# Kernel optimization log

Measured on AMD Instinct MI355X. Metric: run time of the kernel, lower is better.

Reference implementation:

```python
import jax, jax.numpy as jnp
import numpy as np

D_MODEL = 1024
N_HEADS = 16
HEAD_DIM = D_MODEL // N_HEADS
MAX_LEN = 32768
Q_LEN = 16
START_POS = MAX_LEN - Q_LEN
SCALE = 1.0 / np.sqrt(HEAD_DIM)


def setup_inputs() -> dict:
    key = jax.random.key(0)
    ks = jax.random.split(key, 7)
    xav = np.sqrt(6.0 / (D_MODEL + D_MODEL))  # xavier_uniform bound
    return {
        "query": jax.random.normal(ks[0], (Q_LEN, D_MODEL), dtype=jnp.float32),
        "Wq": jax.random.uniform(ks[1], (D_MODEL, D_MODEL), jnp.float32, -xav, xav),
        "Wk": jax.random.uniform(ks[2], (D_MODEL, D_MODEL), jnp.float32, -xav, xav),
        "Wv": jax.random.uniform(ks[3], (D_MODEL, D_MODEL), jnp.float32, -xav, xav),
        "Wo": jax.random.uniform(ks[4], (D_MODEL, D_MODEL), jnp.float32, -xav, xav),
        "cache_k": jax.random.normal(ks[5], (MAX_LEN, N_HEADS, HEAD_DIM), dtype=jnp.float32),
        "cache_v": jax.random.normal(ks[6], (MAX_LEN, N_HEADS, HEAD_DIM), dtype=jnp.float32),
        "start_pos": START_POS,
    }


def reference(query, Wq, Wk, Wv, Wo, cache_k, cache_v, start_pos):
    S = query.shape[0]
    # QKV projections (nn.Linear: y = x @ W.T), reshape to [S, H, hd]
    Q = (query @ Wq.T).reshape(S, N_HEADS, HEAD_DIM)
    K = (query @ Wk.T).reshape(S, N_HEADS, HEAD_DIM)
    V = (query @ Wv.T).reshape(S, N_HEADS, HEAD_DIM)
    # KV-cache update: write new K/V at start_pos, attend over [0, start_pos+S)
    T = start_pos + S  # cached_seq_len (static python int)
    cached_K = jax.lax.dynamic_update_slice(cache_k, K, (start_pos, 0, 0))[:T]
    cached_V = jax.lax.dynamic_update_slice(cache_v, V, (start_pos, 0, 0))[:T]
    # scores: [H, S, T]
    scores = jnp.einsum("shd,thd->hst", Q, cached_K) * jnp.float32(SCALE)
    if T > S:
        # mask key pos j > query row i + start_pos (triu with diagonal=start_pos+1)
        row = jnp.arange(S)[:, None]
        col = jnp.arange(T)[None, :]
        scores = jnp.where(col > row + start_pos, jnp.float32(-jnp.inf), scores)
    attn = jax.nn.softmax(scores, axis=-1)
    out = jnp.einsum("hst,thd->shd", attn, cached_V).reshape(S, D_MODEL)
    output = out @ Wo.T
    return output, K, V
```

## Files before the change

### kernel.cpp

```cpp
#include <hip/hip_runtime.h>

#define D      1024
#define H      16
#define HD     64
#define SP     32752
#define TT     32768
#define SCALE  0.125f
#define NC     128
#define CHUNK  256
#define PSTR   260

__device__ __forceinline__ float4 ldg4(const float* p){ return *reinterpret_cast<const float4*>(p); }
__device__ __forceinline__ void   stg4(float* p, float4 v){ *reinterpret_cast<float4*>(p) = v; }

__device__ __forceinline__ float gemm16_val(const float* __restrict__ x,
                                            const float* __restrict__ W,
                                            int ochunk, int* o_out, int* li_out)
{
    const int t  = threadIdx.x;
    const int o  = ochunk * 16 + (t >> 4);
    const int ds = (t & 15) << 6;

    float4 wv[16];
    const float* wp = W + (size_t)o * D + ds;
    #pragma unroll
    for (int d4 = 0; d4 < 16; ++d4) wv[d4] = ldg4(wp + d4 * 4);

    float a[16];
    #pragma unroll
    for (int i = 0; i < 16; ++i) {
        const float* xp = x + (size_t)i * D + ds;
        float s = 0.f;
        #pragma unroll
        for (int d4 = 0; d4 < 16; ++d4) {
            float4 xv = ldg4(xp + d4 * 4);
            s += wv[d4].x * xv.x + wv[d4].y * xv.y + wv[d4].z * xv.z + wv[d4].w * xv.w;
        }
        a[i] = s;
    }
    #pragma unroll
    for (int off = 8; off >= 1; off >>= 1) {
        #pragma unroll
        for (int i = 0; i < 16; ++i) a[i] += __shfl_xor(a[i], off, 16);
    }
    const int li = t & 15;
    float v = a[0];
    #pragma unroll
    for (int i = 1; i < 16; ++i) v = (li == i) ? a[i] : v;
    *o_out = o; *li_out = li;
    return v;
}

__global__ __launch_bounds__(256) void qkv_proj(
    const float* __restrict__ q,
    const float* __restrict__ Wq, const float* __restrict__ Wk, const float* __restrict__ Wv,
    float* __restrict__ Qws, float* __restrict__ out,
    float* __restrict__ Kn, float* __restrict__ Vn)
{
    const int m      = blockIdx.x >> 6;
    const int ochunk = blockIdx.x & 63;
    const float* W = (m == 0) ? Wq : (m == 1) ? Wk : Wv;
    int o, li;
    float v = gemm16_val(q, W, ochunk, &o, &li);
    if (m == 0) {
        Qws[li * D + o] = v;
    } else if (m == 1) {
        out[16384 + li * D + o] = v;
        Kn[li * D + o] = v;
    } else {
        out[32768 + li * D + o] = v;
        Vn[li * D + o] = v;
    }
}

__global__ __launch_bounds__(256) void out_proj(
    const float* __restrict__ O, const float* __restrict__ Wo, float* __restrict__ out)
{
    int o, li;
    float v = gemm16_val(O, Wo, blockIdx.x, &o, &li);
    out[li * D + o] = v;
}

__global__ __launch_bounds__(256, 4) void attn_partial(
    const float* __restrict__ Qws, const float* __restrict__ K, const float* __restrict__ V,
    const float* __restrict__ Kn, const float* __restrict__ Vn,
    float* __restrict__ num, float* __restrict__ den)
{
    __shared__ float4 q_s[256];
    __shared__ __align__(16) float p_s[16 * PSTR];
    __shared__ float den_s[64];

    const int t     = threadIdx.x;
    const int h     = blockIdx.x & 15;
    const int c     = blockIdx.x >> 4;
    const int cbase = c * CHUNK;

    {
        const int i = t >> 4, d4 = t & 15;
        q_s[t] = ldg4(Qws + (size_t)i * D + h * HD + d4 * 4);
    }
    __syncthreads();

    {
        const int j0 = cbase + t;
        const float* kp = (j0 < SP) ? (K  + (size_t)j0        * D + h * HD)
                                    : (Kn + (size_t)(j0 - SP) * D + h * HD);
        float4 kv[16];
        #pragma unroll
        for (int d4 = 0; d4 < 16; ++d4) kv[d4] = ldg4(kp + d4 * 4);

        if (j0 >= SP) {
            #pragma unroll
            for (int i = 0; i < 16; ++i) {
                float s = 0.f;
                #pragma unroll
                for (int d4 = 0; d4 < 16; ++d4) {
                    float4 qv = q_s[i * 16 + d4];
                    s += kv[d4].x*qv.x + kv[d4].y*qv.y + kv[d4].z*qv.z + kv[d4].w*qv.w;
                }
                p_s[i * PSTR + t] = (j0 <= SP + i) ? __expf(s * SCALE) : 0.f;
            }
        } else {
            #pragma unroll
            for (int i = 0; i < 16; ++i) {
                float s = 0.f;
                #pragma unroll
                for (int d4 = 0; d4 < 16; ++d4) {
                    float4 qv = q_s[i * 16 + d4];
                    s += kv[d4].x*qv.x + kv[d4].y*qv.y + kv[d4].z*qv.z + kv[d4].w*qv.w;
                }
                p_s[i * PSTR + t] = __expf(s * SCALE);
            }
        }
    }
    __syncthreads();

    const int d4 = t & 15, ig = (t >> 4) & 3, jsub = t >> 6;
    float4 a0 = make_float4(0.f,0.f,0.f,0.f), a1 = a0, a2 = a0, a3 = a0;
    float  e0 = 0.f, e1 = 0.f, e2 = 0.f, e3 = 0.f;
    {
        const int jb = jsub * 64;
        const float* vp  = V + (size_t)(cbase + jb) * D + h * HD + d4 * 4;
        const float* p0r = p_s + (4 * ig + 0) * PSTR + jb;
        const float* p1r = p0r + PSTR;
        const float* p2r = p1r + PSTR;
        const float* p3r = p2r + PSTR;

        if (!(c == NC - 1 && jsub == 3)) {
            float4 c0 = ldg4(vp + 0*D), c1 = ldg4(vp + 1*D),
                   c2 = ldg4(vp + 2*D), c3 = ldg4(vp + 3*D);
            #pragma unroll 4
            for (int j = 0; j < 64; j += 4) {
                const float* nx = vp + (size_t)(j + 4) * D;
                float4 n0 = ldg4(nx), n1 = ldg4(nx + D),
                       n2 = ldg4(nx + 2*D), n3 = ldg4(nx + 3*D);
                float4 pA = *reinterpret_cast<const float4*>(p0r + j);
                float4 pB = *reinterpret_cast<const float4*>(p1r + j);
                float4 pC = *reinterpret_cast<const float4*>(p2r + j);
                float4 pD = *reinterpret_cast<const float4*>(p3r + j);
                a0.x += pA.x*c0.x + pA.y*c1.x + pA.z*c2.x + pA.w*c3.x;
                a0.y += pA.x*c0.y + pA.y*c1.y + pA.z*c2.y + pA.w*c3.y;
                a0.z += pA.x*c0.z + pA.y*c1.z + pA.z*c2.z + pA.w*c3.z;
                a0.w += pA.x*c0.w + pA.y*c1.w + pA.z*c2.w + pA.w*c3.w;
                a1.x += pB.x*c0.x + pB.y*c1.x + pB.z*c2.x + pB.w*c3.x;
                a1.y += pB.x*c0.y + pB.y*c1.y + pB.z*c2.y + pB.w*c3.y;
                a1.z += pB.x*c0.z + pB.y*c1.z + pB.z*c2.z + pB.w*c3.z;
                a1.w += pB.x*c0.w + pB.y*c1.w + pB.z*c2.w + pB.w*c3.w;
                a2.x += pC.x*c0.x + pC.y*c1.x + pC.z*c2.x + pC.w*c3.x;
                a2.y += pC.x*c0.y + pC.y*c1.y + pC.z*c2.y + pC.w*c3.y;
                a2.z += pC.x*c0.z + pC.y*c1.z + pC.z*c2.z + pC.w*c3.z;
                a2.w += pC.x*c0.w + pC.y*c1.w + pC.z*c2.w + pC.w*c3.w;
                a3.x += pD.x*c0.x + pD.y*c1.x + pD.z*c2.x + pD.w*c3.x;
                a3.y += pD.x*c0.y + pD.y*c1.y + pD.z*c2.y + pD.w*c3.y;
                a3.z += pD.x*c0.z + pD.y*c1.z + pD.z*c2.z + pD.w*c3.z;
                a3.w += pD.x*c0.w + pD.y*c1.w + pD.z*c2.w + pD.w*c3.w;
                e0 += (pA.x + pA.y) + (pA.z + pA.w);
                e1 += (pB.x + pB.y) + (pB.z + pB.w);
                e2 += (pC.x + pC.y) + (pC.z + pC.w);
                e3 += (pD.x + pD.y) + (pD.z + pD.w);
                c0 = n0; c1 = n1; c2 = n2; c3 = n3;
            }
        } else {
            for (int j = 0; j < 64; ++j) {
                const int jg = cbase + jb + j;
                const float* vr = (jg < SP) ? (vp + (size_t)j * D)
                                            : (Vn + (size_t)(jg - SP) * D + h * HD + d4 * 4);
                float4 vv = ldg4(vr);
                float pa = p0r[j], pb = p1r[j], pc = p2r[j], pd = p3r[j];
                a0.x += pa*vv.x; a0.y += pa*vv.y; a0.z += pa*vv.z; a0.w += pa*vv.w;
                a1.x += pb*vv.x; a1.y += pb*vv.y; a1.z += pb*vv.z; a1.w += pb*vv.w;
                a2.x += pc*vv.x; a2.y += pc*vv.y; a2.z += pc*vv.z; a2.w += pc*vv.w;
                a3.x += pd*vv.x; a3.y += pd*vv.y; a3.z += pd*vv.z; a3.w += pd*vv.w;
                e0 += pa; e1 += pb; e2 += pc; e3 += pd;
            }
        }
    }
    __syncthreads();

    {
        float* ob = p_s + jsub * 1024 + (ig * 16 + d4) * 16;
        stg4(ob + 0,  a0);
        stg4(ob + 4,  a1);
        stg4(ob + 8,  a2);
        stg4(ob + 12, a3);
        if (d4 == 0) {
            den_s[jsub * 16 + ig * 4 + 0] = e0;
            den_s[jsub * 16 + ig * 4 + 1] = e1;
            den_s[jsub * 16 + ig * 4 + 2] = e2;
            den_s[jsub * 16 + ig * 4 + 3] = e3;
        }
    }
    __syncthreads();

    {
        const int i = t >> 4, dq = t & 15;
        const int off = ((i >> 2) * 16 + dq) * 16 + (i & 3) * 4;
        float4 r0 = *reinterpret_cast<const float4*>(p_s + off);
        float4 r1 = *reinterpret_cast<const float4*>(p_s + 1024 + off);
        float4 r2 = *reinterpret_cast<const float4*>(p_s + 2048 + off);
        float4 r3 = *reinterpret_cast<const float4*>(p_s + 3072 + off);
        float4 o;
        o.x = (r0.x + r1.x) + (r2.x + r3.x);
        o.y = (r0.y + r1.y) + (r2.y + r3.y);
        o.z = (r0.z + r1.z) + (r2.z + r3.z);
        o.w = (r0.w + r1.w) + (r2.w + r3.w);
        stg4(num + ((size_t)(h * NC + c) * 16 + i) * 64 + dq * 4, o);
        if (t < 16)
            den[(h * NC + c) * 16 + t] =
                (den_s[t] + den_s[16 + t]) + (den_s[32 + t] + den_s[48 + t]);
    }
}

__global__ __launch_bounds__(256) void combine(
    const float* __restrict__ num, const float* __restrict__ den, float* __restrict__ O)
{
    const int idx = blockIdx.x * 256 + threadIdx.x;
    const int d  = idx & 63;
    const int hh = (idx >> 6) & 15;
    const int i  = idx >> 10;
    float ns = 0.f, ds = 0.f;
    #pragma unroll 8
    for (int c = 0; c < NC; ++c) {
        ns += num[((size_t)(hh * NC + c) * 16 + i) * 64 + d];
        ds += den[(hh * NC + c) * 16 + i];
    }
    O[idx] = ns / ds;
}

extern "C" void kernel_launch(void* const* d_in, const int* in_sizes, int n_in,
                              void* d_out, int out_size, void* d_ws, size_t ws_size,
                              hipStream_t stream)
{
    (void)in_sizes; (void)n_in; (void)out_size; (void)ws_size;
    const float* q  = (const float*)d_in[0];
    const float* Wq = (const float*)d_in[1];
    const float* Wk = (const float*)d_in[2];
    const float* Wv = (const float*)d_in[3];
    const float* Wo = (const float*)d_in[4];
    const float* ck = (const float*)d_in[5];
    const float* cv = (const float*)d_in[6];
    float* out = (float*)d_out;

    float* ws  = (float*)d_ws;
    float* Qws = ws;
    float* Kn  = ws + 16384;
    float* Vn  = ws + 32768;
    float* num = ws + 49152;
    float* den = num + (size_t)16 * NC * 16 * 64;
    float* O   = den + (size_t)16 * NC * 16;

    qkv_proj    <<<192,     256, 0, stream>>>(q, Wq, Wk, Wv, Qws, out, Kn, Vn);
    attn_partial<<<16 * NC, 256, 0, stream>>>(Qws, ck, cv, Kn, Vn, num, den);
    combine     <<<64,      256, 0, stream>>>(num, den, O);
    out_proj    <<<64,      256, 0, stream>>>(O, Wo, out);
}
```

Measured before the change: 392.3 us.

## Stage K tiles through swizzled shared memory for coalesced loads in attn_partial

Replaces the per-thread strided load of a full 64-float K row with cooperative coalesced float4 loads into a rotated (swizzled) shared-memory tile, processed in four 64-key quarters. Each wave then computes scores for four query rows against its key column, reading K from LDS. This is meant to fix uncoalesced global access to the K cache and lower register pressure. In exchange it adds 16KB of LDS and extra barriers, and drops the occupancy hint from the launch bounds.

```diff
diff --git a/kernel.cpp b/kernel.cpp
--- a/kernel.cpp
+++ b/kernel.cpp
@@ -81,11 +81,12 @@
     out[li * D + o] = v;
 }
 
-__global__ __launch_bounds__(256, 4) void attn_partial(
+__global__ __launch_bounds__(256) void attn_partial(
     const float* __restrict__ Qws, const float* __restrict__ K, const float* __restrict__ V,
     const float* __restrict__ Kn, const float* __restrict__ Vn,
     float* __restrict__ num, float* __restrict__ den)
 {
+    __shared__ float4 k_s[1024];
     __shared__ float4 q_s[256];
     __shared__ __align__(16) float p_s[16 * PSTR];
     __shared__ float den_s[64];
@@ -94,6 +95,7 @@
     const int h     = blockIdx.x & 15;
     const int c     = blockIdx.x >> 4;
     const int cbase = c * CHUNK;
+    const int w     = t >> 6, l = t & 63;
 
     {
         const int i = t >> 4, d4 = t & 15;
@@ -101,41 +103,59 @@
     }
     __syncthreads();
 
-    {
-        const int j0 = cbase + t;
-        const float* kp = (j0 < SP) ? (K  + (size_t)j0        * D + h * HD)
-                                    : (Kn + (size_t)(j0 - SP) * D + h * HD);
-        float4 kv[16];
-        #pragma unroll
-        for (int d4 = 0; d4 < 16; ++d4) kv[d4] = ldg4(kp + d4 * 4);
-
-        if (j0 >= SP) {
+    for (int qtr = 0; qtr < 4; ++qtr) {
+        float4 st[4];
+        #pragma unroll
+        for (int k = 0; k < 4; ++k) {
+            const int f  = k * 256 + t;
+            const int jr = f >> 4;
+            const int s  = f & 15;
+            const int jg = cbase + qtr * 64 + jr;
+            const float* src = (jg < SP) ? (K  + (size_t)jg        * D + h * HD + s * 4)
+                                         : (Kn + (size_t)(jg - SP) * D + h * HD + s * 4);
+            st[k] = ldg4(src);
+        }
+        #pragma unroll
+        for (int k = 0; k < 4; ++k) {
+            const int f  = k * 256 + t;
+            const int jr = f >> 4;
+            const int s  = f & 15;
+            k_s[jr * 16 + ((s + jr) & 15)] = st[k];
+        }
+        __syncthreads();
+
+        {
+            const int jcol = qtr * 64 + l;
+            const int jg   = cbase + jcol;
+            float s0 = 0.f, s1 = 0.f, s2 = 0.f, s3 = 0.f;
             #pragma unroll
-            for (int i = 0; i < 16; ++i) {
-                float s = 0.f;
-                #pragma unroll
-                for (int d4 = 0; d4 < 16; ++d4) {
-                    float4 qv = q_s[i * 16 + d4];
-                    s += kv[d4].x*qv.x + kv[d4].y*qv.y + kv[d4].z*qv.z + kv[d4].w*qv.w;
-                }
-                p_s[i * PSTR + t] = (j0 <= SP + i) ? __expf(s * SCALE) : 0.f;
-            }
-        } else {
-            #pragma unroll
-            for (int i = 0; i < 16; ++i) {
-                float s = 0.f;
-                #pragma unroll
-                for (int d4 = 0; d4 < 16; ++d4) {
-                    float4 qv = q_s[i * 16 + d4];
-                    s += kv[d4].x*qv.x + kv[d4].y*qv.y + kv[d4].z*qv.z + kv[d4].w*qv.w;
-                }
-                p_s[i * PSTR + t] = __expf(s * SCALE);
-            }
-        }
-    }
-    __syncthreads();
-
-    const int d4 = t & 15, ig = (t >> 4) & 3, jsub = t >> 6;
+            for (int d4 = 0; d4 < 16; ++d4) {
+                float4 kv = k_s[l * 16 + ((d4 + l) & 15)];
+                float4 q0 = q_s[(w * 4 + 0) * 16 + d4];
+                float4 q1 = q_s[(w * 4 + 1) * 16 + d4];
+                float4 q2 = q_s[(w * 4 + 2) * 16 + d4];
+                float4 q3 = q_s[(w * 4 + 3) * 16 + d4];
+                s0 += kv.x*q0.x + kv.y*q0.y + kv.z*q0.z + kv.w*q0.w;
+                s1 += kv.x*q1.x + kv.y*q1.y + kv.z*q1.z + kv.w*q1.w;
+                s2 += kv.x*q2.x + kv.y*q2.y + kv.z*q2.z + kv.w*q2.w;
+                s3 += kv.x*q3.x + kv.y*q3.y + kv.z*q3.z + kv.w*q3.w;
+            }
+            if (jg >= SP) {
+                p_s[(w*4+0) * PSTR + jcol] = (jg <= SP + w*4+0) ? __expf(s0 * SCALE) : 0.f;
+                p_s[(w*4+1) * PSTR + jcol] = (jg <= SP + w*4+1) ? __expf(s1 * SCALE) : 0.f;
+                p_s[(w*4+2) * PSTR + jcol] = (jg <= SP + w*4+2) ? __expf(s2 * SCALE) : 0.f;
+                p_s[(w*4+3) * PSTR + jcol] = (jg <= SP + w*4+3) ? __expf(s3 * SCALE) : 0.f;
+            } else {
+                p_s[(w*4+0) * PSTR + jcol] = __expf(s0 * SCALE);
+                p_s[(w*4+1) * PSTR + jcol] = __expf(s1 * SCALE);
+                p_s[(w*4+2) * PSTR + jcol] = __expf(s2 * SCALE);
+                p_s[(w*4+3) * PSTR + jcol] = __expf(s3 * SCALE);
+            }
+        }
+        __syncthreads();
+    }
+
+    const int d4 = t & 15, ig = (t >> 4) & 3, jsub = w;
     float4 a0 = make_float4(0.f,0.f,0.f,0.f), a1 = a0, a2 = a0, a3 = a0;
     float  e0 = 0.f, e1 = 0.f, e2 = 0.f, e3 = 0.f;
     {
```

After: 385.6 us. About the same (-1.7%).

## Stage K tiles through swizzled LDS with coalesced loads in QK phase

Applied to the files above, without the earlier changes.

The QK score phase no longer has each thread load a full 256-byte K row into registers. Each wave now loads 16-row K tiles with coalesced float4 accesses, double-buffers them in a swizzled shared array, and each lane computes four query rows against one key. The block-wide barrier between score and PV phases is dropped because each wave appears to consume only its own p_s columns. The launch-bounds occupancy hint is removed and LDS use grows by 32KB, which may reduce occupancy. There is no intra-wave barrier around the LDS buffer reuse, so correctness relies on wave-lockstep execution.

```diff
diff --git a/kernel.cpp b/kernel.cpp
--- a/kernel.cpp
+++ b/kernel.cpp
@@ -81,12 +81,13 @@
     out[li * D + o] = v;
 }
 
-__global__ __launch_bounds__(256, 4) void attn_partial(
+__global__ __launch_bounds__(256) void attn_partial(
     const float* __restrict__ Qws, const float* __restrict__ K, const float* __restrict__ V,
     const float* __restrict__ Kn, const float* __restrict__ Vn,
     float* __restrict__ num, float* __restrict__ den)
 {
     __shared__ float4 q_s[256];
+    __shared__ float4 myk[4][2][256];
     __shared__ __align__(16) float p_s[16 * PSTR];
     __shared__ float den_s[64];
 
@@ -94,6 +95,7 @@
     const int h     = blockIdx.x & 15;
     const int c     = blockIdx.x >> 4;
     const int cbase = c * CHUNK;
+    const int w     = t >> 6, l = t & 63;
 
     {
         const int i = t >> 4, d4 = t & 15;
@@ -102,40 +104,65 @@
     __syncthreads();
 
     {
-        const int j0 = cbase + t;
-        const float* kp = (j0 < SP) ? (K  + (size_t)j0        * D + h * HD)
-                                    : (Kn + (size_t)(j0 - SP) * D + h * HD);
-        float4 kv[16];
+        const int kl    = l & 15;
+        const int qq    = l >> 4;
+        const int kbase = cbase + w * 64;
+        const int row_[4] = { (0*64+l)>>4, (1*64+l)>>4, (2*64+l)>>4, (3*64+l)>>4 };
+        const int sl_ = l & 15;
+
+        float4 st[4];
         #pragma unroll
-        for (int d4 = 0; d4 < 16; ++d4) kv[d4] = ldg4(kp + d4 * 4);
-
-        if (j0 >= SP) {
+        for (int k = 0; k < 4; ++k) {
+            const int jg = kbase + row_[k];
+            const float* src = (jg < SP) ? (K  + (size_t)jg        * D + h * HD + sl_ * 4)
+                                         : (Kn + (size_t)(jg - SP) * D + h * HD + sl_ * 4);
+            st[k] = ldg4(src);
+        }
+
+        for (int s = 0; s < 4; ++s) {
+            const int buf = s & 1;
             #pragma unroll
-            for (int i = 0; i < 16; ++i) {
-                float s = 0.f;
+            for (int k = 0; k < 4; ++k)
+                myk[w][buf][row_[k] * 16 + ((sl_ + row_[k]) & 15)] = st[k];
+            if (s < 3) {
                 #pragma unroll
-                for (int d4 = 0; d4 < 16; ++d4) {
-                    float4 qv = q_s[i * 16 + d4];
-                    s += kv[d4].x*qv.x + kv[d4].y*qv.y + kv[d4].z*qv.z + kv[d4].w*qv.w;
+                for (int k = 0; k < 4; ++k) {
+                    const int jg = kbase + (s + 1) * 16 + row_[k];
+                    const float* src = (jg < SP) ? (K  + (size_t)jg        * D + h * HD + sl_ * 4)
+                                                 : (Kn + (size_t)(jg - SP) * D + h * HD + sl_ * 4);
+                    st[k] = ldg4(src);
                 }
-                p_s[i * PSTR + t] = (j0 <= SP + i) ? __expf(s * SCALE) : 0.f;
-            }
-        } else {
+            }
+            float a0 = 0.f, a1 = 0.f, a2 = 0.f, a3 = 0.f;
             #pragma unroll
-            for (int i = 0; i < 16; ++i) {
-                float s = 0.f;
-                #pragma unroll
-                for (int d4 = 0; d4 < 16; ++d4) {
-                    float4 qv = q_s[i * 16 + d4];
-                    s += kv[d4].x*qv.x + kv[d4].y*qv.y + kv[d4].z*qv.z + kv[d4].w*qv.w;
-                }
-                p_s[i * PSTR + t] = __expf(s * SCALE);
-            }
-        }
-    }
-    __syncthreads();
-
-    const int d4 = t & 15, ig = (t >> 4) & 3, jsub = t >> 6;
+            for (int d4 = 0; d4 < 16; ++d4) {
+                float4 kv = myk[w][buf][kl * 16 + ((d4 + kl) & 15)];
+                float4 q0 = q_s[(qq * 4 + 0) * 16 + d4];
+                float4 q1 = q_s[(qq * 4 + 1) * 16 + d4];
+                float4 q2 = q_s[(qq * 4 + 2) * 16 + d4];
+                float4 q3 = q_s[(qq * 4 + 3) * 16 + d4];
+                a0 += kv.x*q0.x + kv.y*q0.y + kv.z*q0.z + kv.w*q0.w;
+                a1 += kv.x*q1.x + kv.y*q1.y + kv.z*q1.z + kv.w*q1.w;
+                a2 += kv.x*q2.x + kv.y*q2.y + kv.z*q2.z + kv.w*q2.w;
+                a3 += kv.x*q3.x + kv.y*q3.y + kv.z*q3.z + kv.w*q3.w;
+            }
+            const int jcol = w * 64 + s * 16 + kl;
+            const int jg   = cbase + jcol;
+            if (jg >= SP) {
+                p_s[(qq*4+0) * PSTR + jcol] = (jg <= SP + qq*4+0) ? __expf(a0 * SCALE) : 0.f;
+                p_s[(qq*4+1) * PSTR + jcol] = (jg <= SP + qq*4+1) ? __expf(a1 * SCALE) : 0.f;
+                p_s[(qq*4+2) * PSTR + jcol] = (jg <= SP + qq*4+2) ? __expf(a2 * SCALE) : 0.f;
+                p_s[(qq*4+3) * PSTR + jcol] = (jg <= SP + qq*4+3) ? __expf(a3 * SCALE) : 0.f;
+            } else {
+                p_s[(qq*4+0) * PSTR + jcol] = __expf(a0 * SCALE);
+                p_s[(qq*4+1) * PSTR + jcol] = __expf(a1 * SCALE);
+                p_s[(qq*4+2) * PSTR + jcol] = __expf(a2 * SCALE);
+                p_s[(qq*4+3) * PSTR + jcol] = __expf(a3 * SCALE);
+            }
+        }
+    }
+
+    const int d4 = t & 15, ig = (t >> 4) & 3, jsub = w;
     float4 a0 = make_float4(0.f,0.f,0.f,0.f), a1 = a0, a2 = a0, a3 = a0;
     float  e0 = 0.f, e1 = 0.f, e2 = 0.f, e3 = 0.f;
     {
```

After: 380.4 us. -3.0%, faster.
